# Optimization experiments

Measured on AMD Instinct MI355X. Metric: run time of the kernel, lower is better.

The kernel has to match this reference:

```python
import jax, jax.numpy as jnp
import numpy as np

N = 50000        # num nodes
D = 128          # hidden_dim
E = 800000       # num edges (avg_degree = 16)
LN_EPS = 1e-5    # torch LayerNorm default eps


def setup_inputs() -> dict:
    key = jax.random.key(0)
    ks = jax.random.split(key, 8)
    x = jax.random.normal(ks[0], (N, D), dtype=jnp.float32)
    edge_rows = jax.random.randint(ks[1], (E,), 0, N, dtype=jnp.int32)
    edge_cols = jax.random.randint(ks[2], (E,), 0, N, dtype=jnp.int32)
    # Parameters (xavier_uniform for lin1 gain=1.0, lin2 gain=0.5; zero biases)
    lim1 = float(np.sqrt(6.0 / (D + D)))           # gain 1.0
    lim2 = 0.5 * float(np.sqrt(6.0 / (D + D)))     # gain 0.5
    W1 = jax.random.uniform(ks[3], (D, D), minval=-lim1, maxval=lim1, dtype=jnp.float32)
    W2 = jax.random.uniform(ks[4], (D, D), minval=-lim2, maxval=lim2, dtype=jnp.float32)
    b1 = jnp.zeros((D,), dtype=jnp.float32)
    b2 = jnp.zeros((D,), dtype=jnp.float32)
    gamma = jnp.ones((D,), dtype=jnp.float32)      # LayerNorm weight
    beta = jnp.zeros((D,), dtype=jnp.float32)      # LayerNorm bias
    eps = jnp.zeros((), dtype=jnp.float32)         # learnable eps, init 0.0
    return {"x": x, "edge_rows": edge_rows, "edge_cols": edge_cols,
            "W1": W1, "b1": b1, "W2": W2, "b2": b2,
            "gamma": gamma, "beta": beta, "eps": eps}


def layer_norm(x, gamma, beta):
    mu = jnp.mean(x, axis=-1, keepdims=True)
    var = jnp.mean((x - mu) ** 2, axis=-1, keepdims=True)
    return (x - mu) * jax.lax.rsqrt(var + LN_EPS) * gamma + beta


def reference(x, edge_rows, edge_cols, W1, b1, W2, b2, gamma, beta, eps):
    h = layer_norm(x, gamma, beta)                               # [N, D]
    # sparse.mm(adj_t, h): neighbor_sum[i] = sum over edges (i <- j) of h[j]
    neighbor_sum = jax.ops.segment_sum(h[edge_cols], edge_rows, num_segments=N)
    h = (1.0 + eps) * h + neighbor_sum
    h = jax.nn.silu(h @ W1.T + b1)                               # lin1 + SiLU
    h = h @ W2.T + b2                                            # lin2 (dropout p=0 -> identity)
    return x + h
```

## Files before the change

### kernel.cpp

```cpp
#include <hip/hip_runtime.h>
#include <hip/hip_bf16.h>

#define N_NODES 50000
#define DIM 128
#define N_EDGES 800000
#define NBUCKETS 196
#define BINA_EPB 4096
#define BUCKET_CAP 6144

typedef __bf16 bf16_t;
typedef bf16_t bf16x2 __attribute__((ext_vector_type(2)));
typedef bf16_t bf16x4 __attribute__((ext_vector_type(4)));
typedef bf16_t bf16x8 __attribute__((ext_vector_type(8)));
typedef float f32x4 __attribute__((ext_vector_type(4)));

__device__ __forceinline__ float bf_lo(unsigned int u) {
  return __uint_as_float(u << 16);
}
__device__ __forceinline__ float bf_hi(unsigned int u) {
  return __uint_as_float(u & 0xffff0000u);
}

__global__ __launch_bounds__(256) void k_ln(
    const float* __restrict__ x, const float* __restrict__ gamma,
    const float* __restrict__ beta, bf16_t* __restrict__ h,
    int* __restrict__ bcursor) {
  if (blockIdx.x == 0 && threadIdx.x < NBUCKETS) bcursor[threadIdx.x] = 0;
  const int lane = threadIdx.x & 63;
  const int row  = blockIdx.x * 4 + (threadIdx.x >> 6);
  const float2 v = *(const float2*)(x + (size_t)row * DIM + lane * 2);
  float s  = v.x + v.y;
  float ss = v.x * v.x + v.y * v.y;
#pragma unroll
  for (int d = 1; d < 64; d <<= 1) {
    s  += __shfl_xor(s, d);
    ss += __shfl_xor(ss, d);
  }
  const float mu   = s * (1.0f / 128.0f);
  const float var  = ss * (1.0f / 128.0f) - mu * mu;
  const float rstd = rsqrtf(var + 1e-5f);
  const float2 g = *(const float2*)(gamma + lane * 2);
  const float2 b = *(const float2*)(beta + lane * 2);
  const float h0 = (v.x - mu) * rstd * g.x + b.x;
  const float h1 = (v.y - mu) * rstd * g.y + b.y;
  *(bf16x2*)(h + (size_t)row * DIM + lane * 2) = (bf16x2){(bf16_t)h0, (bf16_t)h1};
}

__global__ __launch_bounds__(256) void k_binA(
    const int* __restrict__ erows, const int* __restrict__ ecols,
    int* __restrict__ bcursor, unsigned int* __restrict__ tmp) {
  __shared__ int hist[256];
  const int t = threadIdx.x;
  const int base = blockIdx.x * BINA_EPB;
  hist[t] = 0;
  __syncthreads();
  int bkt[16];
  unsigned int pk[16];
#pragma unroll
  for (int i = 0; i < 16; ++i) {
    const int e = base + i * 256 + t;
    if (e < N_EDGES) {
      const int d = erows[e];
      bkt[i] = d >> 8;
      pk[i] = ((unsigned int)(d & 255) << 16) | (unsigned int)ecols[e];
      atomicAdd(&hist[bkt[i]], 1);
    } else {
      bkt[i] = -1;
    }
  }
  __syncthreads();
  const int cnt = hist[t];
  int g = 0;
  if (t < NBUCKETS && cnt > 0) g = atomicAdd(&bcursor[t], cnt);
  __syncthreads();
  hist[t] = t * BUCKET_CAP + g;
  __syncthreads();
#pragma unroll
  for (int i = 0; i < 16; ++i) {
    if (bkt[i] >= 0) {
      const int pos = atomicAdd(&hist[bkt[i]], 1);
      if (pos < (bkt[i] + 1) * BUCKET_CAP) tmp[pos] = pk[i];
    }
  }
}

__global__ __launch_bounds__(256) void k_binB(
    const unsigned int* __restrict__ tmp, const int* __restrict__ bcursor,
    int* __restrict__ nstart, int* __restrict__ nend,
    unsigned short* __restrict__ sorted) {
  __shared__ int cnt[256];
  __shared__ int cur[256];
  __shared__ int wsum[4];
  const int b = blockIdx.x, t = threadIdx.x;
  const int rs = b * BUCKET_CAP;
  const int re = rs + min(bcursor[b], BUCKET_CAP);
  cnt[t] = 0;
  __syncthreads();
  for (int e = rs + t; e < re; e += 256)
    atomicAdd(&cnt[tmp[e] >> 16], 1);
  __syncthreads();
  const int val = cnt[t];
  const int lane = t & 63, w = t >> 6;
  int v = val;
#pragma unroll
  for (int d = 1; d < 64; d <<= 1) {
    const int n = __shfl_up(v, d);
    if (lane >= d) v += n;
  }
  if (lane == 63) wsum[w] = v;
  __syncthreads();
  int woff = 0;
  for (int k = 0; k < w; ++k) woff += wsum[k];
  const int st = rs + v + woff - val;
  const int nidx = b * 256 + t;
  if (nidx < N_NODES) { nstart[nidx] = st; nend[nidx] = st + val; }
  cur[t] = st;
  __syncthreads();
  for (int e = rs + t; e < re; e += 256) {
    const unsigned int pv = tmp[e];
    const int pos = atomicAdd(&cur[pv >> 16], 1);
    sorted[pos] = (unsigned short)(pv & 0xffffu);
  }
}

__global__ __launch_bounds__(256) void k_gather(
    const uint2* __restrict__ h4, const int* __restrict__ nstart,
    const int* __restrict__ nend, const unsigned short* __restrict__ sorted,
    const float* __restrict__ epsp, bf16_t* __restrict__ acc) {
  const int tid  = threadIdx.x;
  const int lane = tid & 63;
  const int half = lane >> 5;
  const int l31  = lane & 31;
  const int node = blockIdx.x * 4 + (tid >> 6);
  const int s = nstart[node], e = nend[node];
  f32x4 a0 = {0.f, 0.f, 0.f, 0.f};
  f32x4 a1 = {0.f, 0.f, 0.f, 0.f};
  f32x4 a2 = {0.f, 0.f, 0.f, 0.f};
  f32x4 a3 = {0.f, 0.f, 0.f, 0.f};
  for (int base = s; base < e; base += 64) {
    const int cnt = e - base;
    const int m = cnt < 64 ? cnt : 64;
    const int myidx = (lane < m) ? (int)sorted[base + lane] : 0;
    for (int j = 0; j < m; j += 8) {
      const int o0 = j + half;
      const int o1 = j + 2 + half;
      const int o2 = j + 4 + half;
      const int o3 = j + 6 + half;
      const int s0 = __shfl(myidx, o0);
      const int s1 = __shfl(myidx, o1);
      const int s2 = __shfl(myidx, o2);
      const int s3 = __shfl(myidx, o3);
      uint2 v0 = h4[(size_t)s0 * 32 + l31];
      uint2 v1 = h4[(size_t)s1 * 32 + l31];
      uint2 v2 = h4[(size_t)s2 * 32 + l31];
      uint2 v3 = h4[(size_t)s3 * 32 + l31];
      if (o0 >= m) { v0.x = 0u; v0.y = 0u; }
      if (o1 >= m) { v1.x = 0u; v1.y = 0u; }
      if (o2 >= m) { v2.x = 0u; v2.y = 0u; }
      if (o3 >= m) { v3.x = 0u; v3.y = 0u; }
      a0[0] += bf_lo(v0.x); a0[1] += bf_hi(v0.x);
      a0[2] += bf_lo(v0.y); a0[3] += bf_hi(v0.y);
      a1[0] += bf_lo(v1.x); a1[1] += bf_hi(v1.x);
      a1[2] += bf_lo(v1.y); a1[3] += bf_hi(v1.y);
      a2[0] += bf_lo(v2.x); a2[1] += bf_hi(v2.x);
      a2[2] += bf_lo(v2.y); a2[3] += bf_hi(v2.y);
      a3[0] += bf_lo(v3.x); a3[1] += bf_hi(v3.x);
      a3[2] += bf_lo(v3.y); a3[3] += bf_hi(v3.y);
    }
  }
  f32x4 t = (a0 + a1) + (a2 + a3);
#pragma unroll
  for (int k = 0; k < 4; ++k) t[k] += __shfl_xor(t[k], 32);
  if (half == 0) {
    const uint2 hv = h4[(size_t)node * 32 + l31];
    const float epv = 1.0f + epsp[0];
    t[0] += bf_lo(hv.x) * epv; t[1] += bf_hi(hv.x) * epv;
    t[2] += bf_lo(hv.y) * epv; t[3] += bf_hi(hv.y) * epv;
    *(bf16x4*)(acc + (size_t)node * DIM + l31 * 4) =
        (bf16x4){(bf16_t)t[0], (bf16_t)t[1], (bf16_t)t[2], (bf16_t)t[3]};
  }
}

__global__ __launch_bounds__(256) void k_mlp(
    const bf16_t* __restrict__ acc, const float* __restrict__ x,
    const float* __restrict__ W1, const float* __restrict__ b1,
    const float* __restrict__ W2, const float* __restrict__ b2,
    float* __restrict__ out) {
  __shared__ __attribute__((aligned(16))) bf16_t lsA[128 * 136];
  __shared__ __attribute__((aligned(16))) bf16_t lsB[128 * 136];

  const int tid  = threadIdx.x;
  const int lane = tid & 63;
  const int w    = tid >> 6;
  const int l15  = lane & 15;
  const int lq   = lane >> 4;

#pragma unroll
  for (int i = 0; i < 16; ++i) {
    const int idx = i * 1024 + tid * 4;
    const int r = idx >> 7, c = idx & 127;
    const float4 v1 = *(const float4*)(W1 + idx);
    const float4 v2 = *(const float4*)(W2 + idx);
    *(bf16x4*)&lsA[r * 136 + c] =
        (bf16x4){(bf16_t)v1.x, (bf16_t)v1.y, (bf16_t)v1.z, (bf16_t)v1.w};
    *(bf16x4*)&lsB[r * 136 + c] =
        (bf16x4){(bf16_t)v2.x, (bf16_t)v2.y, (bf16_t)v2.z, (bf16_t)v2.w};
  }

  const int rb = blockIdx.x * 128 + w * 32;

  bf16x8 af[2][4];
#pragma unroll
  for (int t = 0; t < 2; ++t)
#pragma unroll
    for (int ks = 0; ks < 4; ++ks) {
      int row = rb + t * 16 + l15;
      row = row < N_NODES ? row : N_NODES - 1;
      af[t][ks] = *(const bf16x8*)(acc + (size_t)row * DIM + ks * 32 + lq * 8);
    }
  __syncthreads();

  f32x4 c1[2][8] = {};
#pragma unroll
  for (int cb = 0; cb < 8; ++cb)
#pragma unroll
    for (int ks = 0; ks < 4; ++ks) {
      const bf16x8 bf = *(const bf16x8*)&lsA[(cb * 16 + l15) * 136 + ks * 32 + lq * 8];
      c1[0][cb] = __builtin_amdgcn_mfma_f32_16x16x32_bf16(af[0][ks], bf, c1[0][cb], 0, 0, 0);
      c1[1][cb] = __builtin_amdgcn_mfma_f32_16x16x32_bf16(af[1][ks], bf, c1[1][cb], 0, 0, 0);
    }
  __syncthreads();

#pragma unroll
  for (int cb = 0; cb < 8; ++cb) {
    const float b1v = b1[cb * 16 + l15];
#pragma unroll
    for (int t = 0; t < 2; ++t)
#pragma unroll
      for (int r = 0; r < 4; ++r) {
        float v = c1[t][cb][r] + b1v;
        v = v / (1.0f + __expf(-v));
        const int ri = w * 32 + t * 16 + lq * 4 + r;
        lsA[ri * 136 + cb * 16 + l15] = (bf16_t)v;
      }
  }
  __syncthreads();

  bf16x8 a2[2][4];
#pragma unroll
  for (int t = 0; t < 2; ++t)
#pragma unroll
    for (int ks = 0; ks < 4; ++ks)
      a2[t][ks] = *(const bf16x8*)&lsA[(w * 32 + t * 16 + l15) * 136 + ks * 32 + lq * 8];

  f32x4 c2[2][8] = {};
#pragma unroll
  for (int cb = 0; cb < 8; ++cb)
#pragma unroll
    for (int ks = 0; ks < 4; ++ks) {
      const bf16x8 bf = *(const bf16x8*)&lsB[(cb * 16 + l15) * 136 + ks * 32 + lq * 8];
      c2[0][cb] = __builtin_amdgcn_mfma_f32_16x16x32_bf16(a2[0][ks], bf, c2[0][cb], 0, 0, 0);
      c2[1][cb] = __builtin_amdgcn_mfma_f32_16x16x32_bf16(a2[1][ks], bf, c2[1][cb], 0, 0, 0);
    }

#pragma unroll
  for (int cb = 0; cb < 8; ++cb) {
    const int c = cb * 16 + l15;
    const float b2v = b2[c];
#pragma unroll
    for (int t = 0; t < 2; ++t)
#pragma unroll
      for (int r = 0; r < 4; ++r) {
        const int row = rb + t * 16 + lq * 4 + r;
        if (row < N_NODES)
          out[(size_t)row * DIM + c] = x[(size_t)row * DIM + c] + c2[t][cb][r] + b2v;
      }
  }
}

extern "C" void kernel_launch(void* const* d_in, const int* in_sizes, int n_in,
                              void* d_out, int out_size, void* d_ws, size_t ws_size,
                              hipStream_t stream) {
  const float* x     = (const float*)d_in[0];
  const int*   erows = (const int*)d_in[1];
  const int*   ecols = (const int*)d_in[2];
  const float* W1    = (const float*)d_in[3];
  const float* b1    = (const float*)d_in[4];
  const float* W2    = (const float*)d_in[5];
  const float* b2    = (const float*)d_in[6];
  const float* gamma = (const float*)d_in[7];
  const float* beta  = (const float*)d_in[8];
  const float* eps   = (const float*)d_in[9];
  float* out = (float*)d_out;

  char* ws = (char*)d_ws;
  bf16_t* h         = (bf16_t*)(ws);
  bf16_t* acc       = (bf16_t*)(ws + 12800000);
  unsigned int* tmp = (unsigned int*)(ws + 12800000);
  unsigned short* sorted = (unsigned short*)(ws + 25600000);
  int*    nstart    = (int*)(ws + 28008448);
  int*    nend      = (int*)(ws + 28208448);
  int*    bcursor   = (int*)(ws + 28408448);

  k_ln    <<<N_NODES / 4, 256, 0, stream>>>(x, gamma, beta, h, bcursor);
  k_binA  <<<(N_EDGES + BINA_EPB - 1) / BINA_EPB, 256, 0, stream>>>(erows, ecols, bcursor, tmp);
  k_binB  <<<NBUCKETS, 256, 0, stream>>>(tmp, bcursor, nstart, nend, sorted);
  k_gather<<<N_NODES / 4, 256, 0, stream>>>((const uint2*)h, nstart, nend, sorted, eps, acc);
  k_mlp   <<<(N_NODES + 127) / 128, 256, 0, stream>>>(acc, x, W1, b1, W2, b2, out);
}
```

Measured before the change: 97.71 us.

## Fuse LayerNorm with edge binning and use per-block bucket segments

```diff
diff --git a/kernel.cpp b/kernel.cpp
--- a/kernel.cpp
+++ b/kernel.cpp
@@ -6,7 +6,10 @@
 #define N_EDGES 800000
 #define NBUCKETS 196
 #define BINA_EPB 4096
+#define NBLKA 196
+#define SEGCAP 64
 #define BUCKET_CAP 6144
+#define LN_BLOCKS 12500
 
 typedef __bf16 bf16_t;
 typedef bf16_t bf16x2 __attribute__((ext_vector_type(2)));
@@ -21,13 +24,51 @@
   return __uint_as_float(u & 0xffff0000u);
 }
 
-__global__ __launch_bounds__(256) void k_ln(
+__global__ __launch_bounds__(256) void k_ln_binA(
     const float* __restrict__ x, const float* __restrict__ gamma,
     const float* __restrict__ beta, bf16_t* __restrict__ h,
-    int* __restrict__ bcursor) {
-  if (blockIdx.x == 0 && threadIdx.x < NBUCKETS) bcursor[threadIdx.x] = 0;
-  const int lane = threadIdx.x & 63;
-  const int row  = blockIdx.x * 4 + (threadIdx.x >> 6);
+    const int* __restrict__ erows, const int* __restrict__ ecols,
+    unsigned int* __restrict__ tmp, int* __restrict__ cnt) {
+  __shared__ int sh_hist[256];
+  __shared__ int sh_cur[256];
+  const int t = threadIdx.x;
+
+  if (blockIdx.x < NBLKA) {
+    const int blk = blockIdx.x;
+    sh_hist[t] = 0;
+    __syncthreads();
+    const int base = blk * BINA_EPB;
+    int bkt[16];
+    unsigned int pk[16];
+#pragma unroll
+    for (int i = 0; i < 16; ++i) {
+      const int e = base + i * 256 + t;
+      if (e < N_EDGES) {
+        const int d = erows[e];
+        bkt[i] = d >> 8;
+        pk[i] = ((unsigned int)(d & 255) << 16) | (unsigned int)ecols[e];
+        atomicAdd(&sh_hist[bkt[i]], 1);
+      } else {
+        bkt[i] = -1;
+      }
+    }
+    __syncthreads();
+    if (t < NBUCKETS) cnt[t * NBLKA + blk] = min(sh_hist[t], SEGCAP);
+    sh_cur[t] = 0;
+    __syncthreads();
+#pragma unroll
+    for (int i = 0; i < 16; ++i) {
+      if (bkt[i] >= 0) {
+        const int pos = atomicAdd(&sh_cur[bkt[i]], 1);
+        if (pos < SEGCAP)
+          tmp[((size_t)bkt[i] * NBLKA + blk) * SEGCAP + pos] = pk[i];
+      }
+    }
+    return;
+  }
+
+  const int lane = t & 63;
+  const int row  = (blockIdx.x - NBLKA) * 4 + (t >> 6);
   const float2 v = *(const float2*)(x + (size_t)row * DIM + lane * 2);
   float s  = v.x + v.y;
   float ss = v.x * v.x + v.y * v.y;
@@ -46,62 +87,19 @@
   *(bf16x2*)(h + (size_t)row * DIM + lane * 2) = (bf16x2){(bf16_t)h0, (bf16_t)h1};
 }
 
-__global__ __launch_bounds__(256) void k_binA(
-    const int* __restrict__ erows, const int* __restrict__ ecols,
-    int* __restrict__ bcursor, unsigned int* __restrict__ tmp) {
-  __shared__ int hist[256];
-  const int t = threadIdx.x;
-  const int base = blockIdx.x * BINA_EPB;
-  hist[t] = 0;
-  __syncthreads();
-  int bkt[16];
-  unsigned int pk[16];
-#pragma unroll
-  for (int i = 0; i < 16; ++i) {
-    const int e = base + i * 256 + t;
-    if (e < N_EDGES) {
-      const int d = erows[e];
-      bkt[i] = d >> 8;
-      pk[i] = ((unsigned int)(d & 255) << 16) | (unsigned int)ecols[e];
-      atomicAdd(&hist[bkt[i]], 1);
-    } else {
-      bkt[i] = -1;
-    }
-  }
-  __syncthreads();
-  const int cnt = hist[t];
-  int g = 0;
-  if (t < NBUCKETS && cnt > 0) g = atomicAdd(&bcursor[t], cnt);
-  __syncthreads();
-  hist[t] = t * BUCKET_CAP + g;
-  __syncthreads();
-#pragma unroll
-  for (int i = 0; i < 16; ++i) {
-    if (bkt[i] >= 0) {
-      const int pos = atomicAdd(&hist[bkt[i]], 1);
-      if (pos < (bkt[i] + 1) * BUCKET_CAP) tmp[pos] = pk[i];
-    }
-  }
-}
-
 __global__ __launch_bounds__(256) void k_binB(
-    const unsigned int* __restrict__ tmp, const int* __restrict__ bcursor,
+    const unsigned int* __restrict__ tmp, const int* __restrict__ cnt,
     int* __restrict__ nstart, int* __restrict__ nend,
     unsigned short* __restrict__ sorted) {
-  __shared__ int cnt[256];
-  __shared__ int cur[256];
+  __shared__ unsigned int stage[BUCKET_CAP];
+  __shared__ int sh_cnt[256];
+  __shared__ int sh_cur[256];
   __shared__ int wsum[4];
   const int b = blockIdx.x, t = threadIdx.x;
-  const int rs = b * BUCKET_CAP;
-  const int re = rs + min(bcursor[b], BUCKET_CAP);
-  cnt[t] = 0;
-  __syncthreads();
-  for (int e = rs + t; e < re; e += 256)
-    atomicAdd(&cnt[tmp[e] >> 16], 1);
-  __syncthreads();
-  const int val = cnt[t];
   const int lane = t & 63, w = t >> 6;
-  int v = val;
+
+  const int c = (t < NBLKA) ? cnt[b * NBLKA + t] : 0;
+  int v = c;
 #pragma unroll
   for (int d = 1; d < 64; d <<= 1) {
     const int n = __shfl_up(v, d);
@@ -111,14 +109,47 @@
   __syncthreads();
   int woff = 0;
   for (int k = 0; k < w; ++k) woff += wsum[k];
-  const int st = rs + v + woff - val;
+  const int soff = v + woff - c;
+  int total = wsum[0] + wsum[1] + wsum[2] + wsum[3];
+  if (total > BUCKET_CAP) total = BUCKET_CAP;
+
+  if (c > 0) {
+    const unsigned int* seg = tmp + ((size_t)b * NBLKA + t) * SEGCAP;
+    for (int j = 0; j < c; ++j) {
+      const int p = soff + j;
+      if (p < BUCKET_CAP) stage[p] = seg[j];
+    }
+  }
+  __syncthreads();
+
+  sh_cnt[t] = 0;
+  __syncthreads();
+  for (int e = t; e < total; e += 256)
+    atomicAdd(&sh_cnt[stage[e] >> 16], 1);
+  __syncthreads();
+
+  const int val = sh_cnt[t];
+  int v2 = val;
+#pragma unroll
+  for (int d = 1; d < 64; d <<= 1) {
+    const int n = __shfl_up(v2, d);
+    if (lane >= d) v2 += n;
+  }
+  __syncthreads();
+  if (lane == 63) wsum[w] = v2;
+  __syncthreads();
+  int woff2 = 0;
+  for (int k = 0; k < w; ++k) woff2 += wsum[k];
+  const int rs = b * BUCKET_CAP;
+  const int st = rs + v2 + woff2 - val;
   const int nidx = b * 256 + t;
   if (nidx < N_NODES) { nstart[nidx] = st; nend[nidx] = st + val; }
-  cur[t] = st;
-  __syncthreads();
-  for (int e = rs + t; e < re; e += 256) {
-    const unsigned int pv = tmp[e];
-    const int pos = atomicAdd(&cur[pv >> 16], 1);
+  sh_cur[t] = st;
+  __syncthreads();
+
+  for (int e = t; e < total; e += 256) {
+    const unsigned int pv = stage[e];
+    const int pos = atomicAdd(&sh_cur[pv >> 16], 1);
     sorted[pos] = (unsigned short)(pv & 0xffffu);
   }
 }
@@ -300,11 +331,11 @@
   unsigned short* sorted = (unsigned short*)(ws + 25600000);
   int*    nstart    = (int*)(ws + 28008448);
   int*    nend      = (int*)(ws + 28208448);
-  int*    bcursor   = (int*)(ws + 28408448);
-
-  k_ln    <<<N_NODES / 4, 256, 0, stream>>>(x, gamma, beta, h, bcursor);
-  k_binA  <<<(N_EDGES + BINA_EPB - 1) / BINA_EPB, 256, 0, stream>>>(erows, ecols, bcursor, tmp);
-  k_binB  <<<NBUCKETS, 256, 0, stream>>>(tmp, bcursor, nstart, nend, sorted);
+  int*    cnt       = (int*)(ws + 28408448);
+
+  k_ln_binA<<<LN_BLOCKS + NBLKA, 256, 0, stream>>>(x, gamma, beta, h,
+                                                   erows, ecols, tmp, cnt);
+  k_binB  <<<NBUCKETS, 256, 0, stream>>>(tmp, cnt, nstart, nend, sorted);
   k_gather<<<N_NODES / 4, 256, 0, stream>>>((const uint2*)h, nstart, nend, sorted, eps, acc);
   k_mlp   <<<(N_NODES + 127) / 128, 256, 0, stream>>>(acc, x, W1, b1, W2, b2, out);
 }
```

New measurement: 88.67 us. 9.2% less time.
